# Optimization experiments

Hardware: AMD Instinct MI355X
Metric: run time of the kernel (lower is better)

The kernel has to match this reference:

```python
import jax, jax.numpy as jnp
import numpy as np

T = 0.07  # temperature from __init__ default


def setup_inputs() -> dict:
    key = jax.random.key(0)
    ks = jax.random.split(key, 5)
    B, D, H, E = 4096, 2048, 2048, 128
    init = lambda k, shp, fan: jax.random.normal(k, shp, dtype=jnp.float32) * (1.0 / np.sqrt(fan))
    return {
        "input1": jax.random.normal(ks[0], (B, D), dtype=jnp.float32),
        "input2": jax.random.normal(ks[1], (B, D), dtype=jnp.float32),
        "W0": init(ks[2], (D, H), D), "b0": jnp.zeros((H,), jnp.float32),
        "W1": init(ks[3], (H, H), H), "b1": jnp.zeros((H,), jnp.float32),
        "W2": init(ks[4], (H, E), H), "b2": jnp.zeros((E,), jnp.float32),
    }


def _mlp(x, W0, b0, W1, b1, W2, b2):
    # Linear -> ReLU -> Linear -> Linear (ReLU only between hidden layers)
    x = jax.nn.relu(x @ W0 + b0)
    x = x @ W1 + b1
    return x @ W2 + b2


def reference(input1, input2, W0, b0, W1, b1, W2, b2):
    B = input1.shape[0]
    e1 = _mlp(input1, W0, b0, W1, b1, W2, b2)
    e2 = _mlp(input2, W0, b0, W1, b1, W2, b2)
    feats = jnp.stack([e1, e2], axis=1)                       # [B, 2, E]
    feats = feats / jnp.linalg.norm(feats, axis=2, keepdims=True)
    # view(N,2,dim).permute(1,0,2).reshape(2N,dim): view0 rows then view1 rows
    f = jnp.concatenate([feats[:, 0], feats[:, 1]], axis=0)   # [2B, E]
    N2 = 2 * B
    sim = (f @ f.T) / T                                        # [2B, 2B]
    idx = jnp.arange(N2)
    pos = sim[idx, (idx + B) % N2]                             # partner view similarity
    # exclude self-similarity (diagonal) from the logsumexp denominator
    sim = jnp.where(jnp.eye(N2, dtype=bool), jnp.float32(-1e9), sim)
    # CE with positive at index 0 of [pos, negatives] == -pos + logsumexp(non-self)
    loss = jnp.mean(jax.nn.logsumexp(sim, axis=1) - pos)
    return loss
```

## Files before the change

### kernel.cpp

```cpp
#include <hip/hip_runtime.h>
#include <stdint.h>

typedef float f32x4 __attribute__((ext_vector_type(4)));
typedef float f32x16 __attribute__((ext_vector_type(16)));
typedef __bf16 bf16x8 __attribute__((ext_vector_type(8)));
typedef unsigned short u16;
typedef unsigned int u32;

#define INVT 14.285714285714286f
#define L2E  1.4426950408889634f

__device__ __forceinline__ u16 f2bf(float f) {
  u32 u = __float_as_uint(f);
  u32 r = (u + 0x7fffu + ((u >> 16) & 1u)) >> 16;
  return (u16)r;
}
__device__ __forceinline__ float bf2f(u16 h) { return __uint_as_float(((u32)h) << 16); }

__device__ __forceinline__ void g2l16(const void* g, void* l) {
  auto gp = reinterpret_cast<__attribute__((address_space(1))) uint32_t*>(
      reinterpret_cast<uintptr_t>(g));
  auto lp = reinterpret_cast<__attribute__((address_space(3))) uint32_t*>(
      reinterpret_cast<uintptr_t>(l));
  __builtin_amdgcn_global_load_lds(gp, lp, 16, 0, 0);
}


__global__ __launch_bounds__(256) void k_prep(const float* __restrict__ in1,
                                              const float* __restrict__ in2,
                                              u16* __restrict__ Xb,
                                              const float* __restrict__ w0, u16* __restrict__ w0t,
                                              const float* __restrict__ w1, u16* __restrict__ w1t,
                                              const float* __restrict__ w2, u16* __restrict__ w2t) {
  const int bid = blockIdx.x;
  const int tid = threadIdx.x;
  if (bid < 2048) {
    __shared__ u16 tl[64][136];
    const int rb = bid >> 4, cb = bid & 15;
    const int R0 = rb * 64, C0 = cb * 128;
    const float* src = (R0 < 4096 ? in1 : in2);
    const int Rs = (R0 < 4096 ? R0 : R0 - 4096);
    const int r = tid >> 2;
    const int cbase = (tid & 3) * 8;
#pragma unroll
    for (int p = 0; p < 4; ++p) {
      const int c = cbase + p * 32;
      const float* sp = src + (size_t)(Rs + r) * 2048 + C0 + c;
      float4 v0 = *(const float4*)sp;
      float4 v1 = *(const float4*)(sp + 4);
      u16* d = &tl[r][c];
      d[0] = f2bf(v0.x); d[1] = f2bf(v0.y); d[2] = f2bf(v0.z); d[3] = f2bf(v0.w);
      d[4] = f2bf(v1.x); d[5] = f2bf(v1.y); d[6] = f2bf(v1.z); d[7] = f2bf(v1.w);
    }
    __syncthreads();
    const int u = tid >> 4, t16 = tid & 15;
    const int g = u >> 3, s = u & 7;
    const int c0 = t16 >> 3, lmb = (t16 & 7) * 4;
    u16* dst = Xb + (size_t)(cb * 8 + s) * 131072 + (rb * 2 + g) * 512 + t16 * 32;
#pragma unroll
    for (int q = 0; q < 4; ++q)
      *(uint4*)(dst + q * 8) = *(const uint4*)&tl[g * 32 + lmb + q][s * 16 + c0 * 8];
    return;
  }
  if (bid < 6144) {
    const int l = tid & 63, w = tid >> 6;
    const int lm = l & 31, ch = l >> 5;
    const int v = (bid - 2048) * 4 + w;
    const int z = v >> 13, u2 = v & 8191;
    const int s = u2 & 127, g = u2 >> 7;
    const float* Wm = z ? w1 : w0;
    u16* O = z ? w1t : w0t;
    const float* src = Wm + (size_t)(s * 16 + ch * 8) * 2048 + g * 32 + lm;
    float f0 = src[0];
    float f1 = src[2048];
    float f2 = src[2 * 2048];
    float f3 = src[3 * 2048];
    float f4 = src[4 * 2048];
    float f5 = src[5 * 2048];
    float f6 = src[6 * 2048];
    float f7 = src[7 * 2048];
    uint4 o;
    o.x = (u32)f2bf(f0) | ((u32)f2bf(f1) << 16);
    o.y = (u32)f2bf(f2) | ((u32)f2bf(f3) << 16);
    o.z = (u32)f2bf(f4) | ((u32)f2bf(f5) << 16);
    o.w = (u32)f2bf(f6) | ((u32)f2bf(f7) << 16);
    *(uint4*)(O + (size_t)s * 32768 + g * 512 + l * 8) = o;
    return;
  }
  __shared__ float t[64][65];
  const int f = bid - 6144;
  const float* in = w2;
  u16* out = w2t;
  const int C = 128, R = 2048;
  const int r0 = (f >> 1) * 64, c0t = (f & 1) * 64;
#pragma unroll
  for (int p = 0; p < 16; ++p) {
    int idx = p * 256 + tid;
    int r = idx >> 6, c = idx & 63;
    t[r][c] = in[(size_t)(r0 + r) * C + (c0t + c)];
  }
  __syncthreads();
#pragma unroll
  for (int p = 0; p < 16; ++p) {
    int idx = p * 256 + tid;
    int c = idx >> 6, r = idx & 63;
    out[(size_t)(c0t + c) * R + (r0 + r)] = f2bf(t[r][c]);
  }
}

__global__ __launch_bounds__(512, 2) void k_gemm(const u16* __restrict__ A, const u16* __restrict__ Bt,
                                                 const float* __restrict__ bias, u16* __restrict__ C,
                                                 int M, int N, int K, int relu, int blockedC) {
  __shared__ __align__(16) u16 sm[65536];
  const int tid = threadIdx.x;
  const int l = tid & 63, w = tid >> 6;
  const int wm = w >> 2, wn = w & 3;
  const int lm = l & 31, c0 = l >> 5;

  const int bid0 = blockIdx.y * 8 + blockIdx.x;
  const int xcd = bid0 & 7, slot = bid0 >> 3;
  const int bx = (xcd & 1) * 4 + (slot & 3);
  const int by = (xcd >> 1) * 8 + (slot >> 2);
  const int m0 = by * 256, n0 = bx * 256;

  const char* gA = (const char*)A + (size_t)((m0 >> 5) + w) * 1024 + l * 16;
  const char* gB = (const char*)Bt + (size_t)((n0 >> 5) + w) * 1024 + l * 16;
  const size_t slabA = (size_t)M * 32, slabB = (size_t)N * 32;

  auto issue_half = [&](int t, int part, int stg) {
    const int h = part >> 1, isB = part & 1;
    const char* g = isB ? gB : gA;
    const size_t slab = isB ? slabB : slabA;
    const int s0 = t * 4 + h * 2;
    char* lb = (char*)sm + stg * 65536 + isB * 32768 + h * 16384 + w * 1024 + l * 16;
    g2l16(g + (size_t)s0 * slab, lb);
    g2l16(g + (size_t)(s0 + 1) * slab, lb + 8192);
  };

  const int fbase = c0 * 256 + lm * 8;
  bf16x8 aX[4], bX[2], aY[4], bY[2];

  auto ldfrag = [&](int buf, int k, bf16x8* a, bf16x8* b) {
    const u16* base = sm + buf * 32768;
    const u16* As = base + (k >> 1) * 8192;
    const u16* Bs = base + 16384 + (k >> 1) * 8192;
    const int fb = (k & 1) * 4096 + fbase;
#pragma unroll
    for (int fm = 0; fm < 4; ++fm)
      a[fm] = *(const bf16x8*)(As + fb + (wm * 4 + fm) * 512);
#pragma unroll
    for (int fn = 0; fn < 2; ++fn)
      b[fn] = *(const bf16x8*)(Bs + fb + (wn * 2 + fn) * 512);
  };

  f32x16 acc[4][2] = {};
  auto mfma8 = [&](bf16x8* a, bf16x8* b) {
    __builtin_amdgcn_s_setprio(1);
#pragma unroll
    for (int fm = 0; fm < 4; ++fm)
#pragma unroll
      for (int fn = 0; fn < 2; ++fn)
        acc[fm][fn] = __builtin_amdgcn_mfma_f32_32x32x16_bf16(a[fm], b[fn],
                                                              acc[fm][fn], 0, 0, 0);
    __builtin_amdgcn_s_setprio(0);
  };

  const int NT = K >> 6;

  issue_half(0, 0, 0); issue_half(0, 1, 0); issue_half(0, 2, 0); issue_half(0, 3, 0);
  asm volatile("s_waitcnt vmcnt(0)" ::: "memory");
  asm volatile("s_barrier" ::: "memory");
  ldfrag(0, 0, aX, bX);

  for (int kt = 0; kt < NT; ++kt) {
    const int buf = kt & 1, nbuf = buf ^ 1;
    const bool pf = (kt + 1) < NT;

    if (pf) { issue_half(kt + 1, 0, nbuf); issue_half(kt + 1, 1, nbuf); }
    ldfrag(buf, 1, aY, bY);
    asm volatile("s_waitcnt lgkmcnt(6)" ::: "memory");
    __builtin_amdgcn_sched_barrier(0);
    mfma8(aX, bX);

    if (pf) { issue_half(kt + 1, 2, nbuf); issue_half(kt + 1, 3, nbuf); }
    ldfrag(buf, 2, aX, bX);
    asm volatile("s_waitcnt lgkmcnt(6)" ::: "memory");
    __builtin_amdgcn_sched_barrier(0);
    mfma8(aY, bY);

    ldfrag(buf, 3, aY, bY);
    asm volatile("s_waitcnt lgkmcnt(6)" ::: "memory");
    __builtin_amdgcn_sched_barrier(0);
    mfma8(aX, bX);

    asm volatile("s_waitcnt lgkmcnt(0)" ::: "memory");
    __builtin_amdgcn_sched_barrier(0);
    mfma8(aY, bY);
    asm volatile("s_waitcnt vmcnt(0)" ::: "memory");
    asm volatile("s_barrier" ::: "memory");
    if (pf) ldfrag(nbuf, 0, aX, bX);
  }

  if (blockedC) {
#pragma unroll
    for (int fn = 0; fn < 2; ++fn) {
      const int col = n0 + wn * 64 + lm + fn * 32;
      const float b = bias[col];
      const int sc = col >> 4, cb = (col >> 3) & 1, e = col & 7;
#pragma unroll
      for (int fm = 0; fm < 4; ++fm) {
        const int gg = (m0 >> 5) + wm * 4 + fm;
        u16* base = C + (size_t)sc * ((size_t)M * 16) + gg * 512 + cb * 256 + e;
#pragma unroll
        for (int g = 0; g < 4; ++g)
#pragma unroll
          for (int rr = 0; rr < 4; ++rr) {
            float v = acc[fm][fn][g * 4 + rr] + b;
            if (relu) v = fmaxf(v, 0.0f);
            base[(4 * c0 + g * 8 + rr) * 8] = f2bf(v);
          }
      }
    }
  } else {
    const int colb = n0 + wn * 64 + lm;
    const int rowb = m0 + wm * 128 + 4 * c0;
#pragma unroll
    for (int fn = 0; fn < 2; ++fn) {
      const float b = bias[colb + fn * 32];
#pragma unroll
      for (int fm = 0; fm < 4; ++fm)
#pragma unroll
        for (int g = 0; g < 4; ++g)
#pragma unroll
          for (int rr = 0; rr < 4; ++rr) {
            float v = acc[fm][fn][g * 4 + rr] + b;
            if (relu) v = fmaxf(v, 0.0f);
            C[(size_t)(rowb + fm * 32 + g * 8 + rr) * N + colb + fn * 32] = f2bf(v);
          }
    }
  }
}

__global__ __launch_bounds__(256, 2) void k_gemm_sk(const u16* __restrict__ A, const u16* __restrict__ Bt,
                                                    float* __restrict__ Ep, int K, int Ksplit) {
  __shared__ __align__(16) u16 sm[24576];
  const int tid = threadIdx.x;
  const int l = tid & 63, w = tid >> 6;
  const int wm = w >> 1, wn = w & 1;
  const int m0 = blockIdx.y * 128;
  const int split = blockIdx.x;
  const int k0s = split * Ksplit;

  const int kb = ((l & 3) ^ ((l >> 3) & 3)) * 16;
  const char* gA = (const char*)(A + (size_t)(m0 + w * 16 + (l >> 2)) * K + k0s) + kb;
  const char* gB = (const char*)(Bt + (size_t)(w * 16 + (l >> 2)) * K + k0s) + kb;
  const size_t radv = (size_t)64 * K * 2;

  auto issue = [&](int kcB, int stg) {
    char* base = (char*)sm + stg * 16384;
    char* dA = base + w * 1024 + l * 16;
    char* dB = base + 8192 + w * 1024 + l * 16;
    g2l16(gA + kcB, dA);
    g2l16(gA + radv + kcB, dA + 4096);
    g2l16(gB + kcB, dB);
    g2l16(gB + radv + kcB, dB + 4096);
  };

  const int lm = l & 31;
  const int c0 = l >> 5;
  const int sw = (lm >> 1) & 3;

  f32x16 acc[2][2] = {};

  auto compute = [&](int stg) {
    const u16* As = sm + stg * 8192;
    const u16* Bs = As + 4096;
#pragma unroll
    for (int t = 0; t < 2; ++t) {
      const int cc = (((t << 1) + c0) ^ sw) * 8;
      bf16x8 a2[2], b2[2];
#pragma unroll
      for (int fm = 0; fm < 2; ++fm) a2[fm] = *(const bf16x8*)(As + (wm * 64 + fm * 32 + lm) * 32 + cc);
#pragma unroll
      for (int fn = 0; fn < 2; ++fn) b2[fn] = *(const bf16x8*)(Bs + (wn * 64 + fn * 32 + lm) * 32 + cc);
#pragma unroll
      for (int fm = 0; fm < 2; ++fm)
#pragma unroll
        for (int fn = 0; fn < 2; ++fn)
          acc[fm][fn] = __builtin_amdgcn_mfma_f32_32x32x16_bf16(a2[fm], b2[fn],
                                                                acc[fm][fn], 0, 0, 0);
    }
  };

  const int NK = Ksplit >> 5;
  issue(0, 0);
  issue(64, 1);
  int st = 0;
  for (int kt = 0; kt < NK; ++kt) {
    if (kt + 1 < NK) asm volatile("s_waitcnt vmcnt(4)" ::: "memory");
    else             asm volatile("s_waitcnt vmcnt(0)" ::: "memory");
    asm volatile("s_barrier" ::: "memory");
    if (kt + 2 < NK) {
      int stp = st + 2; if (stp >= 3) stp -= 3;
      issue((kt + 2) * 64, stp);
    }
    compute(st);
    ++st; if (st == 3) st = 0;
  }

  const int colb = wn * 64 + lm;
  const int rowb = m0 + wm * 64 + 4 * c0;
#pragma unroll
  for (int fn = 0; fn < 2; ++fn)
#pragma unroll
    for (int fm = 0; fm < 2; ++fm)
#pragma unroll
      for (int g = 0; g < 4; ++g)
#pragma unroll
        for (int rr = 0; rr < 4; ++rr)
          Ep[((size_t)split * 8192 + rowb + fm * 32 + g * 8 + rr) * 128 + colb + fn * 32] =
              acc[fm][fn][g * 4 + rr];
}

__global__ __launch_bounds__(256) void k_norm(const float* __restrict__ Ep,
                                              const float* __restrict__ b2, u16* __restrict__ F) {
  const int l = threadIdx.x & 63, w = threadIdx.x >> 6;
  const int row = blockIdx.x * 4 + w;
  const float2* base = (const float2*)Ep + (size_t)row * 64 + l;
  float x = 0.f, y = 0.f;
#pragma unroll
  for (int s = 0; s < 4; ++s) {
    float2 t = base[(size_t)s * (8192 * 64)];
    x += t.x; y += t.y;
  }
  x += b2[l * 2]; y += b2[l * 2 + 1];
  float sq = x * x + y * y;
#pragma unroll
  for (int off = 1; off < 64; off <<= 1) sq += __shfl_xor(sq, off);
  const float inv = 1.0f / sqrtf(sq);
  F[(size_t)row * 128 + l * 2] = f2bf(x * inv);
  F[(size_t)row * 128 + l * 2 + 1] = f2bf(y * inv);
}

__global__ __launch_bounds__(256, 2) void k_sim(const u16* __restrict__ F, float* __restrict__ Sp) {
  __shared__ float red[128];
  const int tid = threadIdx.x;
  const int l = tid & 63, w = tid >> 6;
  const int wm = w >> 1, wn = w & 1;
  const int lm = l & 31, c0 = l >> 5;
  const int r0 = blockIdx.y * 128;
  const int cb0 = blockIdx.x * 1024;

  bf16x8 a[2][8];
#pragma unroll
  for (int fm = 0; fm < 2; ++fm) {
    const int ra = r0 + wm * 64 + fm * 32 + lm;
#pragma unroll
    for (int kf = 0; kf < 8; ++kf)
      a[fm][kf] = *(const bf16x8*)(F + (size_t)ra * 128 + ((kf << 1) + c0) * 8);
  }

  const float S2 = INVT * L2E;
  const int rB = wn * 64 + lm;
  f32x16 runS[2] = {};

#pragma unroll 1
  for (int p = 0; p < 8; ++p) {
    const u16* Fb = F + (size_t)(cb0 + p * 128) * 128;

    f32x16 acc[2][2] = {};
#pragma unroll
    for (int kf = 0; kf < 8; ++kf) {
      const int kc = (kf << 1) + c0;
      bf16x8 b0v = *(const bf16x8*)(Fb + (size_t)rB * 128 + kc * 8);
      bf16x8 b1v = *(const bf16x8*)(Fb + (size_t)(rB + 32) * 128 + kc * 8);
      acc[0][0] = __builtin_amdgcn_mfma_f32_32x32x16_bf16(a[0][kf], b0v, acc[0][0], 0, 0, 0);
      acc[0][1] = __builtin_amdgcn_mfma_f32_32x32x16_bf16(a[0][kf], b1v, acc[0][1], 0, 0, 0);
      acc[1][0] = __builtin_amdgcn_mfma_f32_32x32x16_bf16(a[1][kf], b0v, acc[1][0], 0, 0, 0);
      acc[1][1] = __builtin_amdgcn_mfma_f32_32x32x16_bf16(a[1][kf], b1v, acc[1][1], 0, 0, 0);
    }

    const int cp = cb0 + p * 128;
    if (cp == r0) {
#pragma unroll
      for (int fm = 0; fm < 2; ++fm)
#pragma unroll
        for (int fn = 0; fn < 2; ++fn) {
          const int rcol = wn * 64 + fn * 32 + lm;
#pragma unroll
          for (int r = 0; r < 16; ++r) {
            const int rrow = wm * 64 + fm * 32 + (r & 3) + 8 * (r >> 2) + 4 * c0;
            float e = exp2f(fmaf(acc[fm][fn][r], S2, -S2));
            if (rrow == rcol) e = 0.f;
            runS[fm][r] += e;
          }
        }
    } else {
#pragma unroll
      for (int fm = 0; fm < 2; ++fm)
#pragma unroll
        for (int fn = 0; fn < 2; ++fn)
#pragma unroll
          for (int r = 0; r < 16; ++r)
            runS[fm][r] += exp2f(fmaf(acc[fm][fn][r], S2, -S2));
    }
  }

#pragma unroll
  for (int fm = 0; fm < 2; ++fm)
#pragma unroll
    for (int r = 0; r < 16; ++r) {
      float s = runS[fm][r];
      s += __shfl_xor(s, 1);
      s += __shfl_xor(s, 2);
      s += __shfl_xor(s, 4);
      s += __shfl_xor(s, 8);
      s += __shfl_xor(s, 16);
      runS[fm][r] = s;
    }

  __syncthreads();
  if (wn == 0) {
    if (lm == 0) {
#pragma unroll
      for (int fm = 0; fm < 2; ++fm)
#pragma unroll
        for (int r = 0; r < 16; ++r)
          red[wm * 64 + fm * 32 + (r & 3) + 8 * (r >> 2) + 4 * c0] = runS[fm][r];
    }
  }
  __syncthreads();
  if (wn == 1 && lm == 0) {
#pragma unroll
    for (int fm = 0; fm < 2; ++fm)
#pragma unroll
      for (int r = 0; r < 16; ++r) {
        const int rr = wm * 64 + fm * 32 + (r & 3) + 8 * (r >> 2) + 4 * c0;
        Sp[(size_t)blockIdx.x * 8192 + r0 + rr] = red[rr] + runS[fm][r];
      }
  }
}

__global__ __launch_bounds__(256) void k_combine(const float* __restrict__ Sp,
                                                 const u16* __restrict__ F,
                                                 float* __restrict__ out) {
  const int r = blockIdx.x * 256 + threadIdx.x;
  float S = 0.f;
#pragma unroll
  for (int c = 0; c < 8; ++c) S += Sp[c * 8192 + r];
  const float lse = INVT + logf(S);
  const int par = (r + 4096) & 8191;
  const bf16x8* a = (const bf16x8*)(F + (size_t)r * 128);
  const bf16x8* b = (const bf16x8*)(F + (size_t)par * 128);
  float dot = 0.f;
#pragma unroll
  for (int k = 0; k < 16; ++k) {
    bf16x8 va = a[k], vb = b[k];
#pragma unroll
    for (int j = 0; j < 8; ++j) dot = fmaf((float)va[j], (float)vb[j], dot);
  }
  float contrib = lse - dot * INVT;
#pragma unroll
  for (int off = 1; off < 64; off <<= 1) contrib += __shfl_xor(contrib, off);
  if ((threadIdx.x & 63) == 0) atomicAdd(out, contrib * (1.0f / 8192.0f));
}

extern "C" void kernel_launch(void* const* d_in, const int* in_sizes, int n_in,
                              void* d_out, int out_size, void* d_ws, size_t ws_size,
                              hipStream_t stream) {
  const float* input1 = (const float*)d_in[0];
  const float* input2 = (const float*)d_in[1];
  const float* W0 = (const float*)d_in[2];
  const float* b0 = (const float*)d_in[3];
  const float* W1 = (const float*)d_in[4];
  const float* b1 = (const float*)d_in[5];
  const float* W2 = (const float*)d_in[6];
  const float* b2 = (const float*)d_in[7];
  float* out = (float*)d_out;
  char* ws = (char*)d_ws;

  u16* Xb = (u16*)(ws + 0);
  u16* H1 = (u16*)(ws + 33554432);
  u16* W0T = (u16*)(ws + 67108864);
  u16* W1T = (u16*)(ws + 75497472);
  float* Ep = (float*)(ws + 67108864);
  u16* W2T = (u16*)(ws + 83886080);
  float* Sp = (float*)(ws + 83886080);
  u16* Ff = (u16*)(ws + 84410368);
  u16* H2 = Xb;

  hipMemsetAsync(d_out, 0, sizeof(float), stream);
  k_prep<<<6208, 256, 0, stream>>>(input1, input2, Xb, W0, W0T, W1, W1T, W2, W2T);
  k_gemm<<<dim3(8, 32), 512, 0, stream>>>(Xb, W0T, b0, H1, 8192, 2048, 2048, 1, 1);
  k_gemm<<<dim3(8, 32), 512, 0, stream>>>(H1, W1T, b1, H2, 8192, 2048, 2048, 0, 0);
  k_gemm_sk<<<dim3(4, 64), 256, 0, stream>>>(H2, W2T, Ep, 2048, 512);
  k_norm<<<2048, 256, 0, stream>>>(Ep, b2, Ff);
  k_sim<<<dim3(8, 64), 256, 0, stream>>>(Ff, Sp);
  k_combine<<<32, 256, 0, stream>>>(Sp, Ff, out);
}
```

Before: 336.7 us.

## Shrink split-K GEMM tile to 64 rows, relax k_sim bounds, smaller combine blocks

The third-layer split-K GEMM now uses 64-row tiles with each wave owning a 32-column slice, which doubles the grid to 512 blocks and cuts shared memory and accumulator registers per block. The goal is better occupancy and parallelism on a small GEMM. k_sim drops its min-blocks launch bound, and k_combine runs 128 blocks of 64 threads so more CUs take part. The smaller tiles reload the B operand more often per row, so load traffic per FLOP goes up.

```diff
diff --git a/kernel.cpp b/kernel.cpp
--- a/kernel.cpp
+++ b/kernel.cpp
@@ -243,11 +243,10 @@
 
 __global__ __launch_bounds__(256, 2) void k_gemm_sk(const u16* __restrict__ A, const u16* __restrict__ Bt,
                                                     float* __restrict__ Ep, int K, int Ksplit) {
-  __shared__ __align__(16) u16 sm[24576];
+  __shared__ __align__(16) u16 sm[18432];
   const int tid = threadIdx.x;
   const int l = tid & 63, w = tid >> 6;
-  const int wm = w >> 1, wn = w & 1;
-  const int m0 = blockIdx.y * 128;
+  const int m0 = blockIdx.y * 64;
   const int split = blockIdx.x;
   const int k0s = split * Ksplit;
 
@@ -257,11 +256,10 @@
   const size_t radv = (size_t)64 * K * 2;
 
   auto issue = [&](int kcB, int stg) {
-    char* base = (char*)sm + stg * 16384;
+    char* base = (char*)sm + stg * 12288;
     char* dA = base + w * 1024 + l * 16;
-    char* dB = base + 8192 + w * 1024 + l * 16;
+    char* dB = base + 4096 + w * 1024 + l * 16;
     g2l16(gA + kcB, dA);
-    g2l16(gA + radv + kcB, dA + 4096);
     g2l16(gB + kcB, dB);
     g2l16(gB + radv + kcB, dB + 4096);
   };
@@ -270,25 +268,20 @@
   const int c0 = l >> 5;
   const int sw = (lm >> 1) & 3;
 
-  f32x16 acc[2][2] = {};
+  f32x16 acc[2] = {};
 
   auto compute = [&](int stg) {
-    const u16* As = sm + stg * 8192;
-    const u16* Bs = As + 4096;
+    const u16* As = sm + stg * 6144;
+    const u16* Bs = As + 2048;
 #pragma unroll
     for (int t = 0; t < 2; ++t) {
       const int cc = (((t << 1) + c0) ^ sw) * 8;
-      bf16x8 a2[2], b2[2];
-#pragma unroll
-      for (int fm = 0; fm < 2; ++fm) a2[fm] = *(const bf16x8*)(As + (wm * 64 + fm * 32 + lm) * 32 + cc);
-#pragma unroll
-      for (int fn = 0; fn < 2; ++fn) b2[fn] = *(const bf16x8*)(Bs + (wn * 64 + fn * 32 + lm) * 32 + cc);
-#pragma unroll
-      for (int fm = 0; fm < 2; ++fm)
-#pragma unroll
-        for (int fn = 0; fn < 2; ++fn)
-          acc[fm][fn] = __builtin_amdgcn_mfma_f32_32x32x16_bf16(a2[fm], b2[fn],
-                                                                acc[fm][fn], 0, 0, 0);
+      bf16x8 a2[2], b1;
+#pragma unroll
+      for (int fm = 0; fm < 2; ++fm) a2[fm] = *(const bf16x8*)(As + (fm * 32 + lm) * 32 + cc);
+      b1 = *(const bf16x8*)(Bs + (w * 32 + lm) * 32 + cc);
+      acc[0] = __builtin_amdgcn_mfma_f32_32x32x16_bf16(a2[0], b1, acc[0], 0, 0, 0);
+      acc[1] = __builtin_amdgcn_mfma_f32_32x32x16_bf16(a2[1], b1, acc[1], 0, 0, 0);
     }
   };
 
@@ -297,7 +290,7 @@
   issue(64, 1);
   int st = 0;
   for (int kt = 0; kt < NK; ++kt) {
-    if (kt + 1 < NK) asm volatile("s_waitcnt vmcnt(4)" ::: "memory");
+    if (kt + 1 < NK) asm volatile("s_waitcnt vmcnt(3)" ::: "memory");
     else             asm volatile("s_waitcnt vmcnt(0)" ::: "memory");
     asm volatile("s_barrier" ::: "memory");
     if (kt + 2 < NK) {
@@ -308,18 +301,16 @@
     ++st; if (st == 3) st = 0;
   }
 
-  const int colb = wn * 64 + lm;
-  const int rowb = m0 + wm * 64 + 4 * c0;
-#pragma unroll
-  for (int fn = 0; fn < 2; ++fn)
-#pragma unroll
-    for (int fm = 0; fm < 2; ++fm)
-#pragma unroll
-      for (int g = 0; g < 4; ++g)
-#pragma unroll
-        for (int rr = 0; rr < 4; ++rr)
-          Ep[((size_t)split * 8192 + rowb + fm * 32 + g * 8 + rr) * 128 + colb + fn * 32] =
-              acc[fm][fn][g * 4 + rr];
+  const int colb = w * 32 + lm;
+  const int rowb = m0 + 4 * c0;
+#pragma unroll
+  for (int fm = 0; fm < 2; ++fm)
+#pragma unroll
+    for (int g = 0; g < 4; ++g)
+#pragma unroll
+      for (int rr = 0; rr < 4; ++rr)
+        Ep[((size_t)split * 8192 + rowb + fm * 32 + g * 8 + rr) * 128 + colb] =
+            acc[fm][g * 4 + rr];
 }
 
 __global__ __launch_bounds__(256) void k_norm(const float* __restrict__ Ep,
@@ -342,7 +333,7 @@
   F[(size_t)row * 128 + l * 2 + 1] = f2bf(y * inv);
 }
 
-__global__ __launch_bounds__(256, 2) void k_sim(const u16* __restrict__ F, float* __restrict__ Sp) {
+__global__ __launch_bounds__(256) void k_sim(const u16* __restrict__ F, float* __restrict__ Sp) {
   __shared__ float red[128];
   const int tid = threadIdx.x;
   const int l = tid & 63, w = tid >> 6;
@@ -441,10 +432,10 @@
   }
 }
 
-__global__ __launch_bounds__(256) void k_combine(const float* __restrict__ Sp,
-                                                 const u16* __restrict__ F,
-                                                 float* __restrict__ out) {
-  const int r = blockIdx.x * 256 + threadIdx.x;
+__global__ __launch_bounds__(64) void k_combine(const float* __restrict__ Sp,
+                                                const u16* __restrict__ F,
+                                                float* __restrict__ out) {
+  const int r = blockIdx.x * 64 + threadIdx.x;
   float S = 0.f;
 #pragma unroll
   for (int c = 0; c < 8; ++c) S += Sp[c * 8192 + r];
@@ -493,8 +484,8 @@
   k_prep<<<6208, 256, 0, stream>>>(input1, input2, Xb, W0, W0T, W1, W1T, W2, W2T);
   k_gemm<<<dim3(8, 32), 512, 0, stream>>>(Xb, W0T, b0, H1, 8192, 2048, 2048, 1, 1);
   k_gemm<<<dim3(8, 32), 512, 0, stream>>>(H1, W1T, b1, H2, 8192, 2048, 2048, 0, 0);
-  k_gemm_sk<<<dim3(4, 64), 256, 0, stream>>>(H2, W2T, Ep, 2048, 512);
+  k_gemm_sk<<<dim3(4, 128), 256, 0, stream>>>(H2, W2T, Ep, 2048, 512);
   k_norm<<<2048, 256, 0, stream>>>(Ep, b2, Ff);
   k_sim<<<dim3(8, 64), 256, 0, stream>>>(Ff, Sp);
-  k_combine<<<32, 256, 0, stream>>>(Sp, Ff, out);
-}
+  k_combine<<<128, 64, 0, stream>>>(Sp, Ff, out);
+}
```

New measurement: 348.9 us. +3.6%, slower.
